# Kernel tuning notes

Measured on AMD Instinct MI355X. Metric: run time of the kernel, lower is better.

Reference implementation:

```python
import jax, jax.numpy as jnp
import numpy as np

S0 = 192
C = [16, 32, 48, 64, 80]      # nPlanes = m*i, m=16, 5 strides
SL = [192, 96, 48, 24, 12]    # spatial size per level
OFF27 = jnp.asarray(np.stack(np.meshgrid(*([[-1, 0, 1]] * 3), indexing='ij'), -1).reshape(-1, 3), jnp.int32)
OFF8 = jnp.asarray(np.stack(np.meshgrid(*([[0, 1]] * 3), indexing='ij'), -1).reshape(-1, 3), jnp.int32)


def _flat(c, S):
    return (c[..., 0] * S + c[..., 1]) * S + c[..., 2]


def _grid(coords, S):
    g = jnp.full((S * S * S,), -1, jnp.int32)
    return g.at[_flat(coords, S)].set(jnp.arange(coords.shape[0], dtype=jnp.int32))


def _subconv(feat, coords, grid, S, W):
    # submanifold 3x3x3 conv over active sites only; W: [27, a, b]
    nb = coords[:, None, :] + OFF27                      # [N,27,3]
    valid = jnp.all((nb >= 0) & (nb < S), axis=-1)
    idx = grid[_flat(jnp.clip(nb, 0, S - 1), S)]         # [N,27]
    valid = valid & (idx >= 0)
    g = jnp.where(valid[..., None], feat[jnp.maximum(idx, 0)], 0.0)
    return jnp.einsum('nka,kab->nb', g, W)


def _downconv(feat, grid_f, S_f, out_coords, W):
    # kernel-2 stride-2 sparse conv; W: [8, a, b]
    src = out_coords[:, None, :] * 2 + OFF8              # [M,8,3]
    valid = jnp.all(src < S_f, axis=-1)
    idx = grid_f[_flat(src, S_f)]
    valid = valid & (idx >= 0)
    g = jnp.where(valid[..., None], feat[jnp.maximum(idx, 0)], 0.0)
    return jnp.einsum('nka,kab->nb', g, W)


def _bnrelu(x, g, b, eps=1e-4):
    # BatchNormLeakyReLU(leakiness=0) == BN (batch stats over active sites) + ReLU
    mu = jnp.mean(x, 0)
    var = jnp.mean((x - mu) ** 2, 0)
    return jax.nn.relu((x - mu) * jax.lax.rsqrt(var + eps) * g + b)


def _unpool(feat_c, grid_c, S_c, fine_coords, k):
    # UnPooling x k levels: copy coarse parent feature to each fine active site
    return feat_c[grid_c[_flat(fine_coords // (1 << k), S_c)]]


def _selection(scores):
    return (jax.nn.softmax(scores, axis=1)[:, 1:2] > 0.5).astype(scores.dtype)


def _forward(coords, features, w_in, blk_w, blk_g, blk_b, dn_g, dn_b, dn_w,
             ppn1_w, ppn1_sw, ppn2_w, ppn2_sw, ppn3_w, ppn3_pw, ppn3_sw):
    grids = [_grid(coords[l], SL[l]) for l in range(5)]
    x = _subconv(features, coords[0], grids[0], SL[0], w_in)   # input layer
    fmaps = [x]
    for i in range(4):  # encoder levels with residual blocks + downsample
        for r in range(2):
            h = _bnrelu(x, blk_g[i][2 * r], blk_b[i][2 * r])
            h = _subconv(h, coords[i], grids[i], SL[i], blk_w[i][2 * r])
            h = _bnrelu(h, blk_g[i][2 * r + 1], blk_b[i][2 * r + 1])
            h = _subconv(h, coords[i], grids[i], SL[i], blk_w[i][2 * r + 1])
            x = x + h  # ConcatTable(Identity, conv path) + AddTable, a==b
        x = _downconv(_bnrelu(x, dn_g[i], dn_b[i]), grids[i], SL[i], coords[i + 1], dn_w[i])
        fmaps.append(x)
    x = _subconv(x, coords[4], grids[4], SL[4], ppn1_w)
    ppn1_scores = x @ ppn1_sw                                   # 1x1 conv
    att1 = _unpool(_selection(ppn1_scores), grids[4], SL[4], coords[2], 2)
    y = fmaps[2] * att1                                         # Multiply at half_stride
    y = _subconv(y, coords[2], grids[2], SL[2], ppn2_w)
    ppn2_scores = y @ ppn2_sw
    att2 = _unpool(_selection(ppn2_scores), grids[2], SL[2], coords[0], 2)
    z = fmaps[0] * att2
    z = _subconv(z, coords[0], grids[0], SL[0], ppn3_w)
    out0 = jnp.concatenate([z @ ppn3_pw, z @ ppn3_sw], axis=1)
    out1 = jnp.concatenate([coords[4].astype(out0.dtype), ppn1_scores], axis=1)
    out2 = jnp.concatenate([coords[2].astype(out0.dtype), ppn2_scores], axis=1)
    return out0, out1, out2


def _make_coords():
    rng = np.random.RandomState(0)
    c0 = np.unique(rng.randint(0, S0, size=(100000, 3)), axis=0).astype(np.int32)
    cs = [c0]
    for _ in range(4):
        cs.append(np.unique(cs[-1] // 2, axis=0).astype(np.int32))
    return cs


def setup_inputs():
    key = jax.random.key(0)
    ks = iter(jax.random.split(key, 64))
    cs = _make_coords()
    inp = {f'coords{l}': jnp.asarray(cs[l]) for l in range(5)}
    N0 = cs[0].shape[0]
    inp['features'] = jax.random.normal(next(ks), (N0, 1), jnp.float32)

    def w(k, shape, fan):
        return jax.random.normal(k, shape, jnp.float32) * (fan ** -0.5)

    inp['w_in'] = w(next(ks), (27, 1, C[0]), 27)
    for i in range(4):
        inp[f'blk_w{i}'] = w(next(ks), (4, 27, C[i], C[i]), 27 * C[i])
        inp[f'blk_g{i}'] = jnp.ones((4, C[i]), jnp.float32)
        inp[f'blk_b{i}'] = jnp.zeros((4, C[i]), jnp.float32)
        inp[f'dn_g{i}'] = jnp.ones((C[i],), jnp.float32)
        inp[f'dn_b{i}'] = jnp.zeros((C[i],), jnp.float32)
        inp[f'dn_w{i}'] = w(next(ks), (8, C[i], C[i + 1]), 8 * C[i])
    inp['ppn1_w'] = w(next(ks), (27, C[4], C[4]), 27 * C[4])
    inp['ppn1_sw'] = w(next(ks), (C[4], 2), C[4])
    inp['ppn2_w'] = w(next(ks), (27, C[2], C[2]), 27 * C[2])
    inp['ppn2_sw'] = w(next(ks), (C[2], 2), C[2])
    inp['ppn3_w'] = w(next(ks), (27, C[0], C[0]), 27 * C[0])
    inp['ppn3_pw'] = w(next(ks), (C[0], 3), C[0])
    inp['ppn3_sw'] = w(next(ks), (C[0], 2), C[0])
    return inp


def reference(features, w_in,
              blk_w0, blk_g0, blk_b0, dn_g0, dn_b0, dn_w0,
              blk_w1, blk_g1, blk_b1, dn_g1, dn_b1, dn_w1,
              blk_w2, blk_g2, blk_b2, dn_g2, dn_b2, dn_w2,
              blk_w3, blk_g3, blk_b3, dn_g3, dn_b3, dn_w3,
              ppn1_w, ppn1_sw, ppn2_w, ppn2_sw, ppn3_w, ppn3_pw, ppn3_sw,
              coords0, coords1, coords2, coords3, coords4):
    coords = [coords0, coords1, coords2, coords3, coords4]
    return _forward(coords, features, w_in,
                    [blk_w0, blk_w1, blk_w2, blk_w3],
                    [blk_g0, blk_g1, blk_g2, blk_g3],
                    [blk_b0, blk_b1, blk_b2, blk_b3],
                    [dn_g0, dn_g1, dn_g2, dn_g3],
                    [dn_b0, dn_b1, dn_b2, dn_b3],
                    [dn_w0, dn_w1, dn_w2, dn_w3],
                    ppn1_w, ppn1_sw, ppn2_w, ppn2_sw, ppn3_w, ppn3_pw, ppn3_sw)
```

## Files before the change

### kernel.cpp

```cpp
#include <hip/hip_runtime.h>
#include <cstdint>
#include <cstddef>

#define TPB 256

typedef _Float16 f16x8 __attribute__((ext_vector_type(8)));
typedef float f32x4 __attribute__((ext_vector_type(4)));
typedef const __attribute__((address_space(1))) void* gp1_t;
typedef __attribute__((address_space(3))) void* lp3_t;

__device__ __forceinline__ void block_sync_lds() {
    asm volatile("s_waitcnt lgkmcnt(0)" ::: "memory");
    __builtin_amdgcn_sched_barrier(0);
    __builtin_amdgcn_s_barrier();
    __builtin_amdgcn_sched_barrier(0);
}

template <int N>
__device__ __forceinline__ void waitcnt_vm() {
    asm volatile("s_waitcnt vmcnt(%0)" :: "i"(N) : "memory");
}


static __global__ void kscatter(int* __restrict__ grid, const int* __restrict__ coords,
                                int N, int S) {
    int i = blockIdx.x * blockDim.x + threadIdx.x;
    if (i >= N) return;
    int x = coords[3 * i], y = coords[3 * i + 1], z = coords[3 * i + 2];
    grid[(x * S + y) * S + z] = i;
}

static __global__ void knbr27(int* __restrict__ nbr, const int* __restrict__ coords,
                              const int* __restrict__ grid, int N, int S, int zr) {
    int t = blockIdx.x * blockDim.x + threadIdx.x;
    if (t >= N * 27) return;
    int n = t / 27, k = t - 27 * n;
    int x = coords[3 * n]     + (k / 9) - 1;
    int y = coords[3 * n + 1] + ((k / 3) % 3) - 1;
    int z = coords[3 * n + 2] + (k % 3) - 1;
    int v = -1;
    if ((unsigned)x < (unsigned)S && (unsigned)y < (unsigned)S && (unsigned)z < (unsigned)S)
        v = grid[(x * S + y) * S + z];
    nbr[t] = (v < 0) ? zr : v;
}

static __global__ void kdown8(int* __restrict__ dn, const int* __restrict__ coords,
                              const int* __restrict__ grid, int M, int S_f, int zr) {
    int t = blockIdx.x * blockDim.x + threadIdx.x;
    if (t >= M * 8) return;
    int n = t >> 3, k = t & 7;
    int x = coords[3 * n] * 2     + ((k >> 2) & 1);
    int y = coords[3 * n + 1] * 2 + ((k >> 1) & 1);
    int z = coords[3 * n + 2] * 2 + (k & 1);
    int v = grid[(x * S_f + y) * S_f + z];
    dn[t] = (v < 0) ? zr : v;
}

static __global__ void kup(int* __restrict__ up, const int* __restrict__ cf,
                           const int* __restrict__ gc, int N, int Sc) {
    int n = blockIdx.x * blockDim.x + threadIdx.x;
    if (n >= N) return;
    int x = cf[3 * n] >> 2, y = cf[3 * n + 1] >> 2, z = cf[3 * n + 2] >> 2;
    up[n] = gc[(x * Sc + y) * Sc + z];
}

static __global__ void ksplitw(_Float16* __restrict__ dst, const float* __restrict__ src,
                               int KREAL, int KPAD, int A, int B) {
    int t = blockIdx.x * blockDim.x + threadIdx.x;
    if (t >= KPAD * A * B) return;
    int a = t % A;
    int b = (t / A) % B;
    int k = t / (A * B);
    float v = (k < KREAL) ? src[((size_t)k * A + a) * B + b] : 0.0f;
    _Float16 hi = (_Float16)v;
    _Float16 lo = (_Float16)(v - (float)hi);
    size_t row = ((size_t)k * B + b) * (size_t)(2 * A);
    dst[row + a] = hi;
    dst[row + A + a] = lo;
}


static __global__ void kstats(double* __restrict__ st, const float* __restrict__ x,
                              int N, int C) {
    extern __shared__ double sh[];
    int tid = threadIdx.x;
    int c = tid % C, rl = tid / C;
    double s = 0.0, q = 0.0;
    int base = blockIdx.x * 256 + rl * 64;
    for (int it = 0; it < 64; it++) {
        int r = base + it;
        if (r < N) {
            double v = (double)x[(size_t)r * C + c];
            s += v;
            q = fma(v, v, q);
        }
    }
    double* ss = sh;
    double* sq = sh + 4 * C;
    ss[tid] = s; sq[tid] = q;
    __syncthreads();
    if (tid < C) {
        double S = ss[tid] + ss[tid + C] + ss[tid + 2 * C] + ss[tid + 3 * C];
        double Q = sq[tid] + sq[tid + C] + sq[tid + 2 * C] + sq[tid + 3 * C];
        atomicAdd(&st[tid], S);
        atomicAdd(&st[80 + tid], Q);
    }
}

static __global__ void kbnrelu_h(_Float16* __restrict__ y, const float4* __restrict__ x,
                                 const double* __restrict__ st, const float* __restrict__ g,
                                 const float* __restrict__ b, int N, int C) {
    __shared__ float sc[80], bh[80];
    int tid = threadIdx.x;
    if (tid < C) {
        double invN = 1.0 / (double)N;
        double S = 0.0, Q = 0.0;
#pragma unroll
        for (int c = 0; c < 16; c++) {
            S += st[c * 160 + tid];
            Q += st[c * 160 + 80 + tid];
        }
        double mu = S * invN;
        double var = Q * invN - mu * mu;
        float s = g[tid] * rsqrtf((float)var + 1e-4f);
        sc[tid] = s;
        bh[tid] = b[tid] - (float)mu * s;
    }
    __syncthreads();
    int C8 = C >> 3;
    int chunks = (N + 1) * C8;
    int t = blockIdx.x * blockDim.x + tid;
    if (t >= chunks) return;
    int n = t / C8, cc = t - n * C8;
    f16x8 hi = {}, lo = {};
    if (n < N) {
        float4 q0 = x[n * (C >> 2) + cc * 2];
        float4 q1 = x[n * (C >> 2) + cc * 2 + 1];
        float v[8] = {q0.x, q0.y, q0.z, q0.w, q1.x, q1.y, q1.z, q1.w};
#pragma unroll
        for (int j = 0; j < 8; j++) {
            float r = fmaxf(fmaf(v[j], sc[cc * 8 + j], bh[cc * 8 + j]), 0.0f);
            _Float16 h = (_Float16)r;
            hi[j] = h;
            lo[j] = (_Float16)(r - (float)h);
        }
    }
    *(f16x8*)&y[(size_t)n * 2 * C + cc * 8] = hi;
    *(f16x8*)&y[(size_t)n * 2 * C + C + cc * 8] = lo;
}

static __global__ void kcvt_h(_Float16* __restrict__ y, const float4* __restrict__ x,
                              int N, int C) {
    int C8 = C >> 3;
    int t = blockIdx.x * blockDim.x + threadIdx.x;
    if (t >= (N + 1) * C8) return;
    int n = t / C8, cc = t - n * C8;
    f16x8 hi = {}, lo = {};
    if (n < N) {
        float4 q0 = x[n * (C >> 2) + cc * 2];
        float4 q1 = x[n * (C >> 2) + cc * 2 + 1];
        float v[8] = {q0.x, q0.y, q0.z, q0.w, q1.x, q1.y, q1.z, q1.w};
#pragma unroll
        for (int j = 0; j < 8; j++) {
            _Float16 h = (_Float16)v[j];
            hi[j] = h;
            lo[j] = (_Float16)(v[j] - (float)h);
        }
    }
    *(f16x8*)&y[(size_t)n * 2 * C + cc * 8] = hi;
    *(f16x8*)&y[(size_t)n * 2 * C + C + cc * 8] = lo;
}

static __global__ void kmulatt_h(_Float16* __restrict__ y, const float4* __restrict__ fmap,
                                 const int* __restrict__ up, const float* __restrict__ sc,
                                 int N, int C) {
    int C8 = C >> 3;
    int t = blockIdx.x * blockDim.x + threadIdx.x;
    if (t >= (N + 1) * C8) return;
    int n = t / C8, cc = t - n * C8;
    f16x8 hi = {}, lo = {};
    if (n < N) {
        int p = up[n];
        float att = (sc[2 * p + 1] > sc[2 * p]) ? 1.0f : 0.0f;
        float4 q0 = fmap[n * (C >> 2) + cc * 2];
        float4 q1 = fmap[n * (C >> 2) + cc * 2 + 1];
        float v[8] = {q0.x, q0.y, q0.z, q0.w, q1.x, q1.y, q1.z, q1.w};
#pragma unroll
        for (int j = 0; j < 8; j++) {
            float r = v[j] * att;
            _Float16 h = (_Float16)r;
            hi[j] = h;
            lo[j] = (_Float16)(r - (float)h);
        }
    }
    *(f16x8*)&y[(size_t)n * 2 * C + cc * 8] = hi;
    *(f16x8*)&y[(size_t)n * 2 * C + C + cc * 8] = lo;
}


template <int A, int B, int TAPS, int TPI, int TR, int MT, int KG, bool ADD>
__launch_bounds__(256, 2)
static __global__ void kconvmf(float* __restrict__ out, const _Float16* __restrict__ feat,
                               const int* __restrict__ nbr, const _Float16* __restrict__ Wsp,
                               const float* __restrict__ res, double* __restrict__ stp,
                               int N, int zr) {
    constexpr int NT_W = B / 16;
    static_assert(TR == 4 * MT * 16, "tile/wave mismatch");
    constexpr int KPT = (TPI == 1) ? ((A + 31) & ~31)
                      : (TPI == 2) ? ((A + 15) & ~15)
                                   : ((A + 7) & ~7);
    constexpr int KT = TPI * KPT;
    static_assert(KT % 32 == 0, "KT must be multiple of 32");
    constexpr int KSTEPS = KT / 32;
    constexpr int KTCH = KT / 8;
    constexpr int PKT = (KTCH == 12) ? 16 : KTCH;
    static_assert(PKT == 8 || PKT == 16, "bad PKT");
    constexpr int RH = PKT * 8;
    constexpr int QQ = KPT / 8;
    constexpr int AQ = A / 8;
    constexpr int A2 = 2 * A;
    constexpr int ITERS = (TAPS + TPI - 1) / TPI;
    constexpr int IPG = (ITERS + KG - 1) / KG;
    constexpr int WROWS = 2 * B;
    constexpr int WSBH = WROWS * RH;
    constexpr int WTOT = WROWS * KTCH;
    constexpr int WPT = (WTOT + 255) / 256;
    constexpr int SEGS = MT * KSTEPS * 2;
    constexpr int NWAIT = MT * TPI + WPT;

    __shared__ __attribute__((aligned(16))) _Float16 asb[4 * SEGS * 512];
    __shared__ __attribute__((aligned(16))) _Float16 wsb[WSBH];
    __shared__ double sred[(KG == 1) ? 4 * 2 * B : 1];

    const int tid = threadIdx.x;

    int bx;
    {
        int nwg = gridDim.x, bid = blockIdx.x;
        int q = nwg >> 3, r = nwg & 7, xcd = bid & 7, ix = bid >> 3;
        bx = (xcd < r) ? xcd * (q + 1) + ix : r * (q + 1) + (xcd - r) * q + ix;
    }
    const int row0 = bx * TR;
    const int it0 = (KG > 1) ? blockIdx.y * IPG : 0;
    const int it1 = (KG > 1) ? ((it0 + IPG < ITERS) ? it0 + IPG : ITERS) : ITERS;

    const int lane = tid & 63, wid = tid >> 6;
    const int lrow = lane & 15, lgrp = lane >> 4;
    const int mb = wid * MT * 16;
    const int awb = wid * SEGS * 512;

    int w_lds[WPT], w_off[WPT];
    bool w_ok[WPT], w_real[WPT];
#pragma unroll
    for (int i = 0; i < WPT; i++) {
        int task = tid + i * 256;
        bool ok = (WTOT % 256 == 0) || (task < WTOT);
        int tc = ok ? task : 0;
        int q = tc % KTCH;
        int row = tc / KTCH;
        int bcol = row % B, pp = row / B;
        int t = q / QQ, qq = q - t * QQ;
        w_lds[i] = row * RH + (q ^ (row & (PKT - 1))) * 8;
        w_off[i] = (t * B + bcol) * A2 + pp * A + qq * 8;
        w_ok[i] = ok;
        w_real[i] = ok && (qq < AQ);
    }
    int rowm[MT];
#pragma unroll
    for (int mt = 0; mt < MT; mt++) rowm[mt] = row0 + mb + mt * 16 + lrow;

    f32x4 acc[MT][NT_W];
#pragma unroll
    for (int mt = 0; mt < MT; mt++)
#pragma unroll
        for (int nt = 0; nt < NT_W; nt++)
            acc[mt][nt] = (f32x4){0.f, 0.f, 0.f, 0.f};

    int nidA[MT][TPI], nidB[MT][TPI];
    f16x8 wg[WPT];

    auto loadnbr = [&](auto& nd, int it) {
        int tb = it * TPI;
#pragma unroll
        for (int mt = 0; mt < MT; mt++)
#pragma unroll
            for (int t = 0; t < TPI; t++)
                nd[mt][t] = (rowm[mt] < N && tb + t < TAPS)
                          ? nbr[(size_t)rowm[mt] * TAPS + tb + t] : zr;
    };
    auto issueA = [&](const auto& nd) {
#pragma unroll
        for (int mt = 0; mt < MT; mt++)
#pragma unroll
            for (int ks = 0; ks < KSTEPS; ks++) {
                int qc = ks * 4 + lgrp;
                int t = qc / QQ;
                int cq = qc - t * QQ;
                int id;
                if constexpr (TPI == 1) id = nd[mt][0];
                else if constexpr (TPI == 2) id = (t == 0) ? nd[mt][0] : nd[mt][1];
                else {
                    int lo2 = (t == 0) ? nd[mt][0] : nd[mt][1];
                    int hi2 = (t == 2) ? nd[mt][2] : nd[mt][3];
                    id = (t < 2) ? lo2 : hi2;
                }
                const _Float16* ph;
                const _Float16* pl;
                if constexpr (QQ > AQ) {
                    bool pad = (cq >= AQ);
                    ph = pad ? (feat + (size_t)zr * A2)
                             : (feat + (size_t)id * A2 + cq * 8);
                    pl = pad ? ph : ph + A;
                } else {
                    ph = feat + (size_t)id * A2 + cq * 8;
                    pl = ph + A;
                }
                int sg = (mt * KSTEPS + ks) * 2;
                __builtin_amdgcn_global_load_lds((gp1_t)ph, (lp3_t)&asb[awb + sg * 512], 16, 0, 0);
                __builtin_amdgcn_global_load_lds((gp1_t)pl, (lp3_t)&asb[awb + (sg + 1) * 512], 16, 0, 0);
            }
    };
    auto loadW = [&](int it) {
        size_t base = (size_t)it * TPI * B * A2;
#pragma unroll
        for (int i = 0; i < WPT; i++)
            wg[i] = w_real[i] ? *(const f16x8*)&Wsp[base + w_off[i]] : (f16x8){};
    };
    auto storeW = [&]() {
#pragma unroll
        for (int i = 0; i < WPT; i++)
            if (w_ok[i]) *(f16x8*)&wsb[w_lds[i]] = wg[i];
    };

    loadnbr(nidA, it0);
    issueA(nidA);
    if (it0 + 1 < it1) loadnbr(nidB, it0 + 1);
    loadW(it0);
    storeW();
    block_sync_lds();
    if (it0 + 1 < it1) loadW(it0 + 1);

    auto body = [&](auto& ncur, const auto& nnx, int it) {
        const bool m1 = (it + 1 < it1), m2 = (it + 2 < it1);
        if (m1) waitcnt_vm<NWAIT>(); else waitcnt_vm<0>();
        __builtin_amdgcn_sched_barrier(0);
        f16x8 fh[MT][KSTEPS], fl[MT][KSTEPS];
#pragma unroll
        for (int mt = 0; mt < MT; mt++)
#pragma unroll
            for (int ks = 0; ks < KSTEPS; ks++) {
                int sg = (mt * KSTEPS + ks) * 2;
                fh[mt][ks] = *(const f16x8*)&asb[awb + sg * 512 + lane * 8];
                fl[mt][ks] = *(const f16x8*)&asb[awb + (sg + 1) * 512 + lane * 8];
            }
        asm volatile("s_waitcnt lgkmcnt(0)" ::: "memory");
        __builtin_amdgcn_sched_barrier(0);
        if (m1) issueA(nnx);
        if (m2) loadnbr(ncur, it + 2);
#pragma unroll
        for (int ks = 0; ks < KSTEPS; ++ks) {
            const int qc = ks * 4 + lgrp;
            f16x8 bh[NT_W], bl[NT_W];
#pragma unroll
            for (int nt = 0; nt < NT_W; ++nt) {
                int rH = nt * 16 + lrow;
                bh[nt] = *(const f16x8*)&wsb[rH * RH + (qc ^ (rH & (PKT - 1))) * 8];
                int rL = B + rH;
                bl[nt] = *(const f16x8*)&wsb[rL * RH + (qc ^ (rL & (PKT - 1))) * 8];
            }
#pragma unroll
            for (int mt = 0; mt < MT; ++mt)
#pragma unroll
                for (int nt = 0; nt < NT_W; ++nt) {
                    acc[mt][nt] = __builtin_amdgcn_mfma_f32_16x16x32_f16(fh[mt][ks], bh[nt], acc[mt][nt], 0, 0, 0);
                    acc[mt][nt] = __builtin_amdgcn_mfma_f32_16x16x32_f16(fl[mt][ks], bh[nt], acc[mt][nt], 0, 0, 0);
                    acc[mt][nt] = __builtin_amdgcn_mfma_f32_16x16x32_f16(fh[mt][ks], bl[nt], acc[mt][nt], 0, 0, 0);
                }
        }
        if (m1) {
            block_sync_lds();
            storeW();
            if (m2) loadW(it + 2);
            block_sync_lds();
        }
    };
    for (int it = it0; it < it1; ) {
        body(nidA, nidB, it); ++it;
        if (it >= it1) break;
        body(nidB, nidA, it); ++it;
    }

    const bool dostats = (stp != nullptr);
    double ssum[NT_W], sqs[NT_W];
#pragma unroll
    for (int nt = 0; nt < NT_W; nt++) { ssum[nt] = 0.0; sqs[nt] = 0.0; }
#pragma unroll
    for (int mt = 0; mt < MT; ++mt) {
        int gr0 = row0 + mb + mt * 16 + lgrp * 4;
#pragma unroll
        for (int nt = 0; nt < NT_W; ++nt) {
            int gc = nt * 16 + lrow;
#pragma unroll
            for (int j = 0; j < 4; ++j) {
                int r = gr0 + j;
                if (r < N) {
                    size_t o = (size_t)r * B + gc;
                    if (KG > 1) {
                        atomicAdd(&out[o], acc[mt][nt][j]);
                    } else {
                        float v = acc[mt][nt][j];
                        if (ADD) v += res[o];
                        out[o] = v;
                        if (dostats) {
                            double dv = (double)v;
                            ssum[nt] += dv;
                            sqs[nt] = fma(dv, dv, sqs[nt]);
                        }
                    }
                }
            }
        }
    }
    if (KG == 1) {
        if (dostats) {
#pragma unroll
            for (int nt = 0; nt < NT_W; nt++) {
                ssum[nt] += __shfl_xor(ssum[nt], 16, 64);
                ssum[nt] += __shfl_xor(ssum[nt], 32, 64);
                sqs[nt] += __shfl_xor(sqs[nt], 16, 64);
                sqs[nt] += __shfl_xor(sqs[nt], 32, 64);
            }
            if (lgrp == 0) {
#pragma unroll
                for (int nt = 0; nt < NT_W; nt++) {
                    sred[(wid * 2 + 0) * B + nt * 16 + lrow] = ssum[nt];
                    sred[(wid * 2 + 1) * B + nt * 16 + lrow] = sqs[nt];
                }
            }
            __syncthreads();
            if (wid == 0) {
                double* sb = stp + (bx & 15) * 160;
                for (int c = lane; c < B; c += 64) {
                    double S = sred[c] + sred[2 * B + c] + sred[4 * B + c] + sred[6 * B + c];
                    double Q = sred[B + c] + sred[3 * B + c] + sred[5 * B + c] + sred[7 * B + c];
                    atomicAdd(&sb[c], S);
                    atomicAdd(&sb[80 + c], Q);
                }
            }
        }
    }
}

static __global__ void kconv_in(float* __restrict__ out, const float* __restrict__ f,
                                const int* __restrict__ nbr, const float* __restrict__ W,
                                int N, int zr) {
    int t = blockIdx.x * blockDim.x + threadIdx.x;
    if (t >= N * 4) return;
    int n = t >> 2, bq = t & 3;
    float4 acc = make_float4(0.f, 0.f, 0.f, 0.f);
    const float4* W4 = (const float4*)W;
    for (int k = 0; k < 27; k++) {
        int id = nbr[n * 27 + k];
        if (id == zr) continue;
        float v = f[id];
        float4 w = W4[k * 4 + bq];
        acc.x = fmaf(v, w.x, acc.x);
        acc.y = fmaf(v, w.y, acc.y);
        acc.z = fmaf(v, w.z, acc.z);
        acc.w = fmaf(v, w.w, acc.w);
    }
    ((float4*)out)[n * 4 + bq] = acc;
}


static __global__ void kscores(float* __restrict__ sc, const float* __restrict__ x,
                               const float* __restrict__ w, int N, int C) {
    int n = blockIdx.x * blockDim.x + threadIdx.x;
    if (n >= N) return;
    float s0 = 0.0f, s1 = 0.0f;
    const float* xr = x + (size_t)n * C;
    for (int c = 0; c < C; c++) {
        float v = xr[c];
        s0 = fmaf(v, w[2 * c], s0);
        s1 = fmaf(v, w[2 * c + 1], s1);
    }
    sc[2 * n] = s0;
    sc[2 * n + 1] = s1;
}

static __global__ void kout0(float* __restrict__ out, const float* __restrict__ z,
                             const float* __restrict__ pw, const float* __restrict__ sw,
                             int N) {
    int n = blockIdx.x * blockDim.x + threadIdx.x;
    if (n >= N) return;
    float o0 = 0, o1 = 0, o2 = 0, o3 = 0, o4 = 0;
    const float* zr = z + (size_t)n * 16;
#pragma unroll
    for (int c = 0; c < 16; c++) {
        float v = zr[c];
        o0 = fmaf(v, pw[3 * c], o0);
        o1 = fmaf(v, pw[3 * c + 1], o1);
        o2 = fmaf(v, pw[3 * c + 2], o2);
        o3 = fmaf(v, sw[2 * c], o3);
        o4 = fmaf(v, sw[2 * c + 1], o4);
    }
    float* r = out + (size_t)n * 5;
    r[0] = o0; r[1] = o1; r[2] = o2; r[3] = o3; r[4] = o4;
}

static __global__ void koutc(float* __restrict__ out, const int* __restrict__ coords,
                             const float* __restrict__ sc, int N) {
    int n = blockIdx.x * blockDim.x + threadIdx.x;
    if (n >= N) return;
    float* r = out + (size_t)n * 5;
    r[0] = (float)coords[3 * n];
    r[1] = (float)coords[3 * n + 1];
    r[2] = (float)coords[3 * n + 2];
    r[3] = sc[2 * n];
    r[4] = sc[2 * n + 1];
}


static inline int cdiv(long a, int b) { return (int)((a + b - 1) / b); }

static void conv(hipStream_t s, float* out, const _Float16* feat, const int* nbr,
                 const _Float16* Wsp, const float* res, double* stp,
                 int N, int A, int B, int TAPS, int zr) {
#define CASE(AA, BB, TT, TPI_, TR_, MT_, KG_)                                              \
    else if (A == AA && B == BB && TAPS == TT) {                                           \
        if (KG_ > 1 && !res) hipMemsetAsync(out, 0, (size_t)N * BB * 4, s);                \
        dim3 g(cdiv(N, TR_), KG_), blk(256);                                               \
        if (res) kconvmf<AA, BB, TT, TPI_, TR_, MT_, KG_, true><<<g, blk, 0, s>>>(out, feat, nbr, Wsp, res, stp, N, zr); \
        else     kconvmf<AA, BB, TT, TPI_, TR_, MT_, KG_, false><<<g, blk, 0, s>>>(out, feat, nbr, Wsp, nullptr, stp, N, zr); \
    }
    if (false) {}
    CASE(16, 16, 27,  4, 128,  2, 1)
    CASE(32, 32, 27,  2, 128,  2, 1)
    CASE(48, 48, 27,  2, 128,  2, 1)
    CASE(64, 64, 27,  1, 128,  2, 4)
    CASE(80, 80, 27,  1,  64,  1, 9)
    CASE(16, 32,  8,  4, 128,  2, 1)
    CASE(32, 48,  8,  2, 128,  2, 1)
    CASE(48, 64,  8,  2,  64,  1, 2)
    CASE(64, 80,  8,  1,  64,  1, 2)
#undef CASE
}

static void bnapply(hipStream_t s, _Float16* out, const float* x, double* st,
                    const float* g, const float* b, int N, int C, bool pre) {
    if (!pre)
        kstats<<<cdiv(N, 256), 4 * C, 8 * C * 2 * sizeof(double), s>>>(st, x, N, C);
    int chunks = (N + 1) * (C / 8);
    kbnrelu_h<<<cdiv(chunks, 256), 256, 0, s>>>(out, (const float4*)x, st, g, b, N, C);
}

extern "C" void kernel_launch(void* const* d_in, const int* in_sizes, int n_in,
                              void* d_out, int out_size, void* d_ws, size_t ws_size,
                              hipStream_t stream) {
    (void)n_in; (void)out_size; (void)ws_size;
    const int SL[5] = {192, 96, 48, 24, 12};
    const int C[5] = {16, 32, 48, 64, 80};
    int N[5];
    const int* coords[5];
    for (int l = 0; l < 5; l++) { N[l] = in_sizes[l] / 3; coords[l] = (const int*)d_in[l]; }
    const float* features = (const float*)d_in[5];
    const float* w_in = (const float*)d_in[6];
    const float *blk_w[4], *blk_g[4], *blk_b[4], *dn_g[4], *dn_b[4], *dn_w[4];
    for (int i = 0; i < 4; i++) {
        blk_w[i] = (const float*)d_in[7 + 6 * i];
        blk_g[i] = (const float*)d_in[8 + 6 * i];
        blk_b[i] = (const float*)d_in[9 + 6 * i];
        dn_g[i] = (const float*)d_in[10 + 6 * i];
        dn_b[i] = (const float*)d_in[11 + 6 * i];
        dn_w[i] = (const float*)d_in[12 + 6 * i];
    }
    const float* ppn1_w  = (const float*)d_in[31];
    const float* ppn1_sw = (const float*)d_in[32];
    const float* ppn2_w  = (const float*)d_in[33];
    const float* ppn2_sw = (const float*)d_in[34];
    const float* ppn3_w  = (const float*)d_in[35];
    const float* ppn3_pw = (const float*)d_in[36];
    const float* ppn3_sw = (const float*)d_in[37];
    float* dout = (float*)d_out;

    char* ws = (char*)d_ws;
    size_t off = 0;
    auto alloc = [&](size_t bytes) -> char* {
        off = (off + 255) & ~(size_t)255;
        char* p = ws + off;
        off += bytes;
        return p;
    };
    int* nbr[5];
    for (int l = 0; l < 5; l++) nbr[l] = (int*)alloc((size_t)N[l] * 27 * 4);
    int* down8[4];
    for (int i = 0; i < 4; i++) down8[i] = (int*)alloc((size_t)N[i + 1] * 8 * 4);
    int* up1 = (int*)alloc((size_t)N[2] * 4);
    int* up2 = (int*)alloc((size_t)N[0] * 4);
    double* stats = (double*)alloc((size_t)26 * 2560 * sizeof(double));
    _Float16* blkWsp[4];
    _Float16* dnWsp[4];
    for (int i = 0; i < 4; i++) {
        blkWsp[i] = (_Float16*)alloc((size_t)4 * 28 * C[i] * 2 * C[i] * 2);
        dnWsp[i] = (_Float16*)alloc((size_t)8 * C[i + 1] * 2 * C[i] * 2);
    }
    _Float16* p1Wsp = (_Float16*)alloc((size_t)27 * 80 * 160 * 2);
    _Float16* p2Wsp = (_Float16*)alloc((size_t)28 * 48 * 96 * 2);
    _Float16* p3Wsp = (_Float16*)alloc((size_t)28 * 16 * 32 * 2);
    float* fmap0 = (float*)alloc((size_t)N[0] * 16 * 4);
    float* fmap2 = (float*)alloc((size_t)N[2] * 48 * 4);
    float* sc1 = (float*)alloc((size_t)N[4] * 2 * 4);
    float* sc2 = (float*)alloc((size_t)N[2] * 2 * 4);

    size_t BIG = 0;
    for (int l = 0; l < 5; l++) {
        size_t s = (size_t)(N[l] + 1) * C[l] * 4;
        if (s > BIG) BIG = s;
    }
    BIG = (BIG + 255) & ~(size_t)255;
    off = (off + 255) & ~(size_t)255;
    size_t trans = off;
    int* grid[5];
    size_t gtot = 0;
    for (int l = 0; l < 5; l++) {
        grid[l] = (int*)(ws + trans + gtot);
        gtot += (size_t)SL[l] * SL[l] * SL[l] * 4;
    }
    float* B0 = (float*)(ws + trans);
    float* B1 = (float*)(ws + trans + BIG);
    float* B2 = (float*)(ws + trans + 2 * BIG);

    hipMemsetAsync(ws + trans, 0xFF, gtot, stream);
    hipMemsetAsync(stats, 0, (size_t)26 * 2560 * sizeof(double), stream);
    for (int l = 0; l < 5; l++)
        kscatter<<<cdiv(N[l], TPB), TPB, 0, stream>>>(grid[l], coords[l], N[l], SL[l]);
    for (int l = 0; l < 5; l++)
        knbr27<<<cdiv((long)N[l] * 27, TPB), TPB, 0, stream>>>(nbr[l], coords[l], grid[l], N[l], SL[l], N[l]);
    for (int i = 0; i < 4; i++)
        kdown8<<<cdiv((long)N[i + 1] * 8, TPB), TPB, 0, stream>>>(down8[i], coords[i + 1], grid[i], N[i + 1], SL[i], N[i]);
    kup<<<cdiv(N[2], TPB), TPB, 0, stream>>>(up1, coords[2], grid[4], N[2], 12);
    kup<<<cdiv(N[0], TPB), TPB, 0, stream>>>(up2, coords[0], grid[2], N[0], 48);
    for (int i = 0; i < 4; i++) {
        int Ci = C[i];
        for (int c = 0; c < 4; c++) {
            int n1 = 28 * Ci * Ci;
            ksplitw<<<cdiv(n1, TPB), TPB, 0, stream>>>(
                blkWsp[i] + (size_t)c * 28 * Ci * 2 * Ci,
                blk_w[i] + (size_t)c * 27 * Ci * Ci, 27, 28, Ci, Ci);
        }
        int n2 = 8 * Ci * C[i + 1];
        ksplitw<<<cdiv(n2, TPB), TPB, 0, stream>>>(dnWsp[i], dn_w[i], 8, 8, Ci, C[i + 1]);
    }
    ksplitw<<<cdiv(28 * 6400, TPB), TPB, 0, stream>>>(p1Wsp, ppn1_w, 27, 27, 80, 80);
    ksplitw<<<cdiv(28 * 2304, TPB), TPB, 0, stream>>>(p2Wsp, ppn2_w, 27, 28, 48, 48);
    ksplitw<<<cdiv(28 * 256, TPB), TPB, 0, stream>>>(p3Wsp, ppn3_w, 27, 28, 16, 16);

    int slot = 0;
    auto stn = [&]() { return stats + 2560 * (slot++); };
    auto stpeek = [&]() { return stats + 2560 * slot; };

    float* curX = B0;
    kconv_in<<<cdiv((long)N[0] * 4, TPB), TPB, 0, stream>>>(curX, features, nbr[0], w_in, N[0], N[0]);
    hipMemcpyAsync(fmap0, curX, (size_t)N[0] * 16 * 4, hipMemcpyDeviceToDevice, stream);

    auto others = [&](float* cur, float*& t1, float*& t2) {
        if (cur == B0) { t1 = B1; t2 = B2; }
        else if (cur == B1) { t1 = B0; t2 = B2; }
        else { t1 = B0; t2 = B1; }
    };

    bool entryPre = false;
    for (int i = 0; i < 4; i++) {
        int Ni = N[i], Ci = C[i];
        float *T1, *T2;
        others(curX, T1, T2);
        size_t wsl = (size_t)28 * Ci * 2 * Ci;
        bool fuseL = (i < 3);
        for (int r = 0; r < 2; r++) {
            bnapply(stream, (_Float16*)T1, curX, stn(), blk_g[i] + (2 * r) * Ci,
                    blk_b[i] + (2 * r) * Ci, Ni, Ci, r == 0 ? entryPre : fuseL);
            conv(stream, T2, (const _Float16*)T1, nbr[i], blkWsp[i] + (2 * r) * wsl,
                 nullptr, fuseL ? stpeek() : nullptr, Ni, Ci, Ci, 27, Ni);
            bnapply(stream, (_Float16*)T1, T2, stn(), blk_g[i] + (2 * r + 1) * Ci,
                    blk_b[i] + (2 * r + 1) * Ci, Ni, Ci, fuseL);
            conv(stream, curX, (const _Float16*)T1, nbr[i], blkWsp[i] + (2 * r + 1) * wsl,
                 curX, fuseL ? stpeek() : nullptr, Ni, Ci, Ci, 27, Ni);
        }
        bnapply(stream, (_Float16*)T1, curX, stn(), dn_g[i], dn_b[i], Ni, Ci, fuseL);
        bool fuseD = (i < 2);
        conv(stream, T2, (const _Float16*)T1, down8[i], dnWsp[i], nullptr,
             fuseD ? stpeek() : nullptr, N[i + 1], Ci, C[i + 1], 8, Ni);
        entryPre = fuseD;
        if (i == 1)
            hipMemcpyAsync(fmap2, T2, (size_t)N[2] * 48 * 4, hipMemcpyDeviceToDevice, stream);
        curX = T2;
    }

    float *T1, *T2;
    others(curX, T1, T2);
    kcvt_h<<<cdiv((N[4] + 1) * 10, TPB), TPB, 0, stream>>>((_Float16*)T1, (const float4*)curX, N[4], 80);
    conv(stream, T2, (const _Float16*)T1, nbr[4], p1Wsp, nullptr, nullptr, N[4], 80, 80, 27, N[4]);
    kscores<<<cdiv(N[4], TPB), TPB, 0, stream>>>(sc1, T2, ppn1_sw, N[4], 80);
    koutc<<<cdiv(N[4], TPB), TPB, 0, stream>>>(dout + (size_t)N[0] * 5, coords[4], sc1, N[4]);
    kmulatt_h<<<cdiv((long)(N[2] + 1) * 6, TPB), TPB, 0, stream>>>((_Float16*)curX, (const float4*)fmap2, up1, sc1, N[2], 48);
    conv(stream, T1, (const _Float16*)curX, nbr[2], p2Wsp, nullptr, nullptr, N[2], 48, 48, 27, N[2]);
    kscores<<<cdiv(N[2], TPB), TPB, 0, stream>>>(sc2, T1, ppn2_sw, N[2], 48);
    koutc<<<cdiv(N[2], TPB), TPB, 0, stream>>>(dout + (size_t)(N[0] + N[4]) * 5, coords[2], sc2, N[2]);
    kmulatt_h<<<cdiv((long)(N[0] + 1) * 2, TPB), TPB, 0, stream>>>((_Float16*)T2, (const float4*)fmap0, up2, sc2, N[0], 16);
    conv(stream, curX, (const _Float16*)T2, nbr[0], p3Wsp, nullptr, nullptr, N[0], 16, 16, 27, N[0]);
    kout0<<<cdiv(N[0], TPB), TPB, 0, stream>>>(dout, curX, ppn3_pw, ppn3_sw, N[0]);
}
```

Before: 1.316 ms.

## Replace async global-to-LDS gather with direct register loads, shrink tiles

Removes the asynchronous global_load_lds staging of gathered neighbor features through LDS. The A-operand fragments are now loaded straight into registers with ordinary vector loads, and the next iteration's loads are issued after the current MFMAs. This drops the LDS round trip and the vmcnt/lgkmcnt waits, but the explicit overlap of gather latency with compute is lost and now depends on compiler scheduling and occupancy. To compensate, most conv configs drop to 64-row tiles with MT=1, and one downconv gets more K-groups, which raises block count and occupancy.

```diff
diff --git a/kernel.cpp b/kernel.cpp
--- a/kernel.cpp
+++ b/kernel.cpp
@@ -6,19 +6,12 @@
 
 typedef _Float16 f16x8 __attribute__((ext_vector_type(8)));
 typedef float f32x4 __attribute__((ext_vector_type(4)));
-typedef const __attribute__((address_space(1))) void* gp1_t;
-typedef __attribute__((address_space(3))) void* lp3_t;
 
 __device__ __forceinline__ void block_sync_lds() {
     asm volatile("s_waitcnt lgkmcnt(0)" ::: "memory");
     __builtin_amdgcn_sched_barrier(0);
     __builtin_amdgcn_s_barrier();
     __builtin_amdgcn_sched_barrier(0);
-}
-
-template <int N>
-__device__ __forceinline__ void waitcnt_vm() {
-    asm volatile("s_waitcnt vmcnt(%0)" :: "i"(N) : "memory");
 }
 
 
@@ -225,10 +218,7 @@
     constexpr int WSBH = WROWS * RH;
     constexpr int WTOT = WROWS * KTCH;
     constexpr int WPT = (WTOT + 255) / 256;
-    constexpr int SEGS = MT * KSTEPS * 2;
-    constexpr int NWAIT = MT * TPI + WPT;
-
-    __shared__ __attribute__((aligned(16))) _Float16 asb[4 * SEGS * 512];
+
     __shared__ __attribute__((aligned(16))) _Float16 wsb[WSBH];
     __shared__ double sred[(KG == 1) ? 4 * 2 * B : 1];
 
@@ -247,7 +237,6 @@
     const int lane = tid & 63, wid = tid >> 6;
     const int lrow = lane & 15, lgrp = lane >> 4;
     const int mb = wid * MT * 16;
-    const int awb = wid * SEGS * 512;
 
     int w_lds[WPT], w_off[WPT];
     bool w_ok[WPT], w_real[WPT];
@@ -277,6 +266,7 @@
             acc[mt][nt] = (f32x4){0.f, 0.f, 0.f, 0.f};
 
     int nidA[MT][TPI], nidB[MT][TPI];
+    f16x8 fa[MT][KSTEPS][2];
     f16x8 wg[WPT];
 
     auto loadnbr = [&](auto& nd, int it) {
@@ -288,7 +278,7 @@
                 nd[mt][t] = (rowm[mt] < N && tb + t < TAPS)
                           ? nbr[(size_t)rowm[mt] * TAPS + tb + t] : zr;
     };
-    auto issueA = [&](const auto& nd) {
+    auto loadA = [&](const auto& nd) {
 #pragma unroll
         for (int mt = 0; mt < MT; mt++)
 #pragma unroll
@@ -304,20 +294,15 @@
                     int hi2 = (t == 2) ? nd[mt][2] : nd[mt][3];
                     id = (t < 2) ? lo2 : hi2;
                 }
-                const _Float16* ph;
-                const _Float16* pl;
+                const _Float16* p = feat + (size_t)id * A2 + cq * 8;
                 if constexpr (QQ > AQ) {
-                    bool pad = (cq >= AQ);
-                    ph = pad ? (feat + (size_t)zr * A2)
-                             : (feat + (size_t)id * A2 + cq * 8);
-                    pl = pad ? ph : ph + A;
+                    bool okc = (cq < AQ);
+                    fa[mt][ks][0] = okc ? *(const f16x8*)p : (f16x8){};
+                    fa[mt][ks][1] = okc ? *(const f16x8*)(p + A) : (f16x8){};
                 } else {
-                    ph = feat + (size_t)id * A2 + cq * 8;
-                    pl = ph + A;
+                    fa[mt][ks][0] = *(const f16x8*)p;
+                    fa[mt][ks][1] = *(const f16x8*)(p + A);
                 }
-                int sg = (mt * KSTEPS + ks) * 2;
-                __builtin_amdgcn_global_load_lds((gp1_t)ph, (lp3_t)&asb[awb + sg * 512], 16, 0, 0);
-                __builtin_amdgcn_global_load_lds((gp1_t)pl, (lp3_t)&asb[awb + (sg + 1) * 512], 16, 0, 0);
             }
     };
     auto loadW = [&](int it) {
@@ -331,32 +316,7 @@
         for (int i = 0; i < WPT; i++)
             if (w_ok[i]) *(f16x8*)&wsb[w_lds[i]] = wg[i];
     };
-
-    loadnbr(nidA, it0);
-    issueA(nidA);
-    if (it0 + 1 < it1) loadnbr(nidB, it0 + 1);
-    loadW(it0);
-    storeW();
-    block_sync_lds();
-    if (it0 + 1 < it1) loadW(it0 + 1);
-
-    auto body = [&](auto& ncur, const auto& nnx, int it) {
-        const bool m1 = (it + 1 < it1), m2 = (it + 2 < it1);
-        if (m1) waitcnt_vm<NWAIT>(); else waitcnt_vm<0>();
-        __builtin_amdgcn_sched_barrier(0);
-        f16x8 fh[MT][KSTEPS], fl[MT][KSTEPS];
-#pragma unroll
-        for (int mt = 0; mt < MT; mt++)
-#pragma unroll
-            for (int ks = 0; ks < KSTEPS; ks++) {
-                int sg = (mt * KSTEPS + ks) * 2;
-                fh[mt][ks] = *(const f16x8*)&asb[awb + sg * 512 + lane * 8];
-                fl[mt][ks] = *(const f16x8*)&asb[awb + (sg + 1) * 512 + lane * 8];
-            }
-        asm volatile("s_waitcnt lgkmcnt(0)" ::: "memory");
-        __builtin_amdgcn_sched_barrier(0);
-        if (m1) issueA(nnx);
-        if (m2) loadnbr(ncur, it + 2);
+    auto domfma = [&]() {
 #pragma unroll
         for (int ks = 0; ks < KSTEPS; ++ks) {
             const int qc = ks * 4 + lgrp;
@@ -372,11 +332,26 @@
             for (int mt = 0; mt < MT; ++mt)
 #pragma unroll
                 for (int nt = 0; nt < NT_W; ++nt) {
-                    acc[mt][nt] = __builtin_amdgcn_mfma_f32_16x16x32_f16(fh[mt][ks], bh[nt], acc[mt][nt], 0, 0, 0);
-                    acc[mt][nt] = __builtin_amdgcn_mfma_f32_16x16x32_f16(fl[mt][ks], bh[nt], acc[mt][nt], 0, 0, 0);
-                    acc[mt][nt] = __builtin_amdgcn_mfma_f32_16x16x32_f16(fh[mt][ks], bl[nt], acc[mt][nt], 0, 0, 0);
+                    acc[mt][nt] = __builtin_amdgcn_mfma_f32_16x16x32_f16(fa[mt][ks][0], bh[nt], acc[mt][nt], 0, 0, 0);
+                    acc[mt][nt] = __builtin_amdgcn_mfma_f32_16x16x32_f16(fa[mt][ks][1], bh[nt], acc[mt][nt], 0, 0, 0);
+                    acc[mt][nt] = __builtin_amdgcn_mfma_f32_16x16x32_f16(fa[mt][ks][0], bl[nt], acc[mt][nt], 0, 0, 0);
                 }
         }
+    };
+
+    loadnbr(nidA, it0);
+    loadA(nidA);
+    loadW(it0);
+    storeW();
+    if (it0 + 1 < it1) loadnbr(nidB, it0 + 1);
+    block_sync_lds();
+    if (it0 + 1 < it1) loadW(it0 + 1);
+
+    auto body = [&](auto& ncur, const auto& nnx, int it) {
+        const bool m1 = (it + 1 < it1), m2 = (it + 2 < it1);
+        domfma();
+        if (m1) loadA(nnx);
+        if (m2) loadnbr(ncur, it + 2);
         if (m1) {
             block_sync_lds();
             storeW();
@@ -534,15 +509,15 @@
         else     kconvmf<AA, BB, TT, TPI_, TR_, MT_, KG_, false><<<g, blk, 0, s>>>(out, feat, nbr, Wsp, nullptr, stp, N, zr); \
     }
     if (false) {}
-    CASE(16, 16, 27,  4, 128,  2, 1)
-    CASE(32, 32, 27,  2, 128,  2, 1)
-    CASE(48, 48, 27,  2, 128,  2, 1)
-    CASE(64, 64, 27,  1, 128,  2, 4)
+    CASE(16, 16, 27,  4,  64,  1, 1)
+    CASE(32, 32, 27,  2,  64,  1, 1)
+    CASE(48, 48, 27,  2,  64,  1, 1)
+    CASE(64, 64, 27,  1,  64,  1, 4)
     CASE(80, 80, 27,  1,  64,  1, 9)
-    CASE(16, 32,  8,  4, 128,  2, 1)
-    CASE(32, 48,  8,  2, 128,  2, 1)
+    CASE(16, 32,  8,  4,  64,  1, 1)
+    CASE(32, 48,  8,  2,  64,  1, 1)
     CASE(48, 64,  8,  2,  64,  1, 2)
-    CASE(64, 80,  8,  1,  64,  1, 2)
+    CASE(64, 80,  8,  1,  64,  1, 4)
 #undef CASE
 }
 
```

Result: faster. 1.245 ms, median of 2 (-5.4%).
